# Performance work log

Measured on AMD Instinct MI355X. Metric: run time of the kernel, lower is better.

The kernel has to match this reference:

```python
import jax, jax.numpy as jnp
import numpy as np

CELL = 16          # pixels_per_cell
ORI = 6            # orientations
BIN_W = 180.0 / ORI
EPS = 1e-5         # skimage block-norm eps


def setup_inputs() -> dict:
    key = jax.random.key(0)
    x = jax.random.normal(key, (32, 3, 512, 512), dtype=jnp.float32)
    return {"x": x}


def _hog(x):
    # x: (B, 3, H, W) -> per-image HOG feature vector, matching skimage.feature.hog
    img = jnp.transpose(x, (0, 2, 3, 1))
    gray = 0.299 * img[..., 0] + 0.587 * img[..., 1] + 0.114 * img[..., 2]  # (B,H,W)
    B, H, W = gray.shape

    # skimage central-difference gradients with zeroed borders
    g_row = jnp.zeros_like(gray).at[:, 1:-1, :].set(gray[:, 2:, :] - gray[:, :-2, :])
    g_col = jnp.zeros_like(gray).at[:, :, 1:-1].set(gray[:, :, 2:] - gray[:, :, :-2])

    mag = jnp.hypot(g_row, g_col)
    ori = jnp.degrees(jnp.arctan2(g_row, g_col)) % 180.0
    bins = jnp.clip(jnp.floor(ori / BIN_W).astype(jnp.int32), 0, ORI - 1)

    # hard-assigned orientation histogram per 16x16 cell, averaged over cell pixels
    weighted = jax.nn.one_hot(bins, ORI, dtype=mag.dtype) * mag[..., None]  # (B,H,W,ORI)
    ncr, ncc = H // CELL, W // CELL
    cells = weighted.reshape(B, ncr, CELL, ncc, CELL, ORI).sum(axis=(2, 4)) / (CELL * CELL)

    # 2x2-cell blocks with stride 1 cell: (B, nbr, nbc, 2, 2, ORI)
    blocks = jnp.stack(
        [jnp.stack([cells[:, :-1, :-1], cells[:, :-1, 1:]], axis=3),
         jnp.stack([cells[:, 1:, :-1], cells[:, 1:, 1:]], axis=3)],
        axis=3)

    # L2-Hys normalization
    n1 = jnp.sqrt(jnp.sum(blocks * blocks, axis=(3, 4, 5), keepdims=True) + EPS * EPS)
    nb = jnp.minimum(blocks / n1, 0.2)
    n2 = jnp.sqrt(jnp.sum(nb * nb, axis=(3, 4, 5), keepdims=True) + EPS * EPS)
    nb = nb / n2
    return nb.reshape(B, -1).astype(jnp.float32)


def reference(x):
    return _hog(x)
```

## Files before the change

kernel.cpp:

```cpp
#include <hip/hip_runtime.h>
#include <math.h>

#define BATCH 32
#define HH 512
#define WW 512
#define NC 32
#define NORI 6
#define CH 262144

__device__ __forceinline__ int bin_of(float a) {
    const float deg = __fmul_rn(a, 57.29577951308232f);
    float m = fmodf(deg, 180.0f);
    if (m < 0.0f) m = __fadd_rn(m, 180.0f);
    const int b = (int)floorf(__fdiv_rn(m, 30.0f));
    return min(max(b, 0), NORI - 1);
}
__device__ __forceinline__ float ulp_step(float x, int k) {
    const int i = __float_as_int(x);
    int key = (i >= 0) ? i : -(i & 0x7FFFFFFF);
    key += k;
    const int r = (key >= 0) ? key : (int)(0x80000000u | (unsigned)(-key));
    return __int_as_float(r);
}
__device__ __forceinline__ void deposit(float acc[NORI], int bin, float val) {
#pragma unroll
    for (int o = 0; o < NORI; ++o) acc[o] += (bin == o) ? val : 0.0f;
}
__device__ __forceinline__ float gray_i(const float* __restrict__ img, int off) {
    return __fadd_rn(__fadd_rn(__fmul_rn(0.299f, img[off]),
                               __fmul_rn(0.587f, img[off + CH])),
                     __fmul_rn(0.114f, img[off + 2 * CH]));
}

__global__ __launch_bounds__(256) void hog_cells_kernel(const float* __restrict__ x,
                                                        float* __restrict__ cells) {
    const int b = blockIdx.z;
    const int tid = threadIdx.x;
    const int wave = tid >> 6, lane = tid & 63;
    const int R0 = blockIdx.y * 64 + wave * 16;
    const int cbase = blockIdx.x * 64;
    const int c = cbase + lane;
    const float* img = x + (size_t)b * 3 * HH * WW;

    const bool is_edge = (lane == 0) || (lane == 63);
    int hc = (lane == 0) ? (cbase - 1) : (cbase + 64);
    hc = min(max(hc, 0), WW - 1);

    float gm1 = gray_i(img, max(R0 - 1, 0) * WW + c);
    float g0  = gray_i(img, R0 * WW + c);
    float hcur = is_edge ? gray_i(img, R0 * WW + hc) : 0.0f;

    const float CC = 0.86602540378443864676f, SS = 0.5f, EPS = 1e-5f;
    const bool col_ok = (c >= 1) && (c < WW - 1);
    float acc[NORI] = {0, 0, 0, 0, 0, 0};
    unsigned ambmask = 0;

#pragma unroll
    for (int k = 0; k < 16; ++k) {
        const int r = R0 + k;
        const int rn = min(r + 1, HH - 1);
        const float gp1 = gray_i(img, rn * WW + c);
        const float hnext = is_edge ? gray_i(img, rn * WW + hc) : 0.0f;

        const bool row_ok = (r >= 1) && (r < HH - 1);
        const float gy = row_ok ? __fsub_rn(gp1, gm1) : 0.0f;
        float gl = __shfl(g0, (lane + 63) & 63);
        float gr = __shfl(g0, (lane + 1) & 63);
        if (lane == 0)  gl = hcur;
        if (lane == 63) gr = hcur;
        const float gx = col_ok ? __fsub_rn(gr, gl) : 0.0f;

        const float mag = __fsqrt_rn(__fmaf_rn(gy, gy, __fmul_rn(gx, gx)));
        const bool neg = gy < 0.0f;
        const float cy = fabsf(gy);
        const float cx = neg ? -gx : gx;
        const float t1 = __fmaf_rn(cy, CC, -__fmul_rn(cx, SS));
        const float t2 = __fmaf_rn(cy, SS, -__fmul_rn(cx, CC));
        const float t3 = -cx;
        const float t4 = __fmaf_rn(cy, -SS, -__fmul_rn(cx, CC));
        const float t5 = __fmaf_rn(cy, -CC, -__fmul_rn(cx, SS));
        int bin = (t1 >= 0.0f) + (t2 >= 0.0f) + (t3 >= 0.0f) +
                  (t4 >= 0.0f) + (t5 >= 0.0f);
        const float s = __fmul_rn(mag, EPS);
        const float mn = fminf(fminf(fminf(fabsf(t1), fabsf(t2)),
                                     fminf(fabsf(t3), fabsf(t4))), fabsf(t5));
        bool amb = (mn < s) || (cx < 0.0f && cy < s);
        if (gy == 0.0f) { bin = 0; amb = false; }
        else if (gx == 0.0f) { bin = 3; amb = false; }

        ambmask |= amb ? (1u << k) : 0u;
        deposit(acc, bin, amb ? 0.0f : mag);

        gm1 = g0; g0 = gp1; hcur = hnext;
    }

    if (__any(ambmask != 0)) {
        unsigned m = ambmask;
        while (m) {
            const int k = __builtin_ctz(m);
            m &= m - 1;
            const int r = R0 + k;
            const int off = r * WW + c;
            const float gy = __fsub_rn(gray_i(img, off + WW), gray_i(img, off - WW));
            const float gx = __fsub_rn(gray_i(img, off + 1), gray_i(img, off - 1));
            const float mag = __fsqrt_rn(__fmaf_rn(gy, gy, __fmul_rn(gx, gx)));
            const float a = atan2f(gy, gx);
            const int bl = bin_of(ulp_step(a, -2));
            const int bh = bin_of(ulp_step(a, +2));
            if (bl == bh) {
                deposit(acc, bl, mag);
            } else {
                const int b0 = bin_of(a);
                const int bo = (b0 == bl) ? bh : bl;
                deposit(acc, b0, __fmul_rn(mag, 0.65f));
                deposit(acc, bo, __fmul_rn(mag, 0.35f));
            }
        }
    }

#pragma unroll
    for (int o = 0; o < NORI; ++o) {
        float v = acc[o];
        v += __shfl_xor(v, 1);
        v += __shfl_xor(v, 2);
        v += __shfl_xor(v, 4);
        v += __shfl_xor(v, 8);
        acc[o] = v;
    }
    if ((lane & 15) == 0) {
        const int cell_r = R0 >> 4;
        const int cell_c = (cbase >> 4) + (lane >> 4);
        float* cp = cells + (((size_t)b * NC + cell_r) * NC + cell_c) * NORI;
#pragma unroll
        for (int o = 0; o < NORI; ++o) cp[o] = acc[o] * (1.0f / 256.0f);
    }
}

__global__ __launch_bounds__(256) void hog_norm_kernel(const float* __restrict__ cells,
                                                       float* __restrict__ out) {
    const int idx = blockIdx.x * 256 + threadIdx.x;
    const int total = BATCH * 31 * 31;
    if (idx >= total) return;
    const int bc = idx % 31;
    const int t = idx / 31;
    const int br = t % 31;
    const int b = t / 31;

    const float* cb = cells + (size_t)b * NC * NC * NORI;
    const float2* p0 = (const float2*)(cb + ((br) * NC + bc) * NORI);
    const float2* p1 = (const float2*)(cb + ((br + 1) * NC + bc) * NORI);
    float v[24];
#pragma unroll
    for (int q = 0; q < 6; ++q) {
        const float2 r0 = p0[q], r1 = p1[q];
        v[2 * q] = r0.x; v[2 * q + 1] = r0.y;
        v[12 + 2 * q] = r1.x; v[12 + 2 * q + 1] = r1.y;
    }
    float ss = 0.0f;
#pragma unroll
    for (int k = 0; k < 24; ++k) ss = __fadd_rn(ss, __fmul_rn(v[k], v[k]));
    const float n1 = __fsqrt_rn(__fadd_rn(ss, 1e-10f));
    float ss2 = 0.0f;
#pragma unroll
    for (int k = 0; k < 24; ++k) {
        v[k] = fminf(__fdiv_rn(v[k], n1), 0.2f);
        ss2 = __fadd_rn(ss2, __fmul_rn(v[k], v[k]));
    }
    const float n2 = __fsqrt_rn(__fadd_rn(ss2, 1e-10f));
    float* op = out + (size_t)idx * 24;
#pragma unroll
    for (int k = 0; k < 24; ++k) op[k] = __fdiv_rn(v[k], n2);
}

extern "C" void kernel_launch(void* const* d_in, const int* in_sizes, int n_in,
                              void* d_out, int out_size, void* d_ws, size_t ws_size,
                              hipStream_t stream) {
    const float* x = (const float*)d_in[0];
    float* out = (float*)d_out;
    float* cells = (float*)d_ws;

    dim3 g1(8, 8, BATCH), b1(256);
    hog_cells_kernel<<<g1, b1, 0, stream>>>(x, cells);

    const int total = BATCH * 31 * 31;
    hog_norm_kernel<<<(total + 255) / 256, 256, 0, stream>>>(cells, out);
}
```

Before: 153.2 us.

## Vectorize gray loads to float4 and retile cells with shared-memory reduction

Each lane now handles 4 adjacent columns and loads RGB through float4. Each block covers one 16-row cell row across 256 columns, with each wave taking 4 rows. Per-cell histograms are reduced with shared-memory atomics instead of a full 16-row per-wave loop, and the grid changes to 2x32xB. This widens global loads and shortens the serial row loop, at the cost of shared atomics, an extra sync, and more halo row loads per output (two extra rows for every four).

```diff
diff --git a/kernel.cpp b/kernel.cpp
--- a/kernel.cpp
+++ b/kernel.cpp
@@ -26,10 +26,50 @@
 #pragma unroll
     for (int o = 0; o < NORI; ++o) acc[o] += (bin == o) ? val : 0.0f;
 }
+__device__ __forceinline__ float gray_comb(float r, float g, float b) {
+    return __fadd_rn(__fadd_rn(__fmul_rn(0.299f, r), __fmul_rn(0.587f, g)),
+                     __fmul_rn(0.114f, b));
+}
 __device__ __forceinline__ float gray_i(const float* __restrict__ img, int off) {
-    return __fadd_rn(__fadd_rn(__fmul_rn(0.299f, img[off]),
-                               __fmul_rn(0.587f, img[off + CH])),
-                     __fmul_rn(0.114f, img[off + 2 * CH]));
+    return gray_comb(img[off], img[off + CH], img[off + 2 * CH]);
+}
+__device__ __forceinline__ float4 gray4(const float* __restrict__ img, int off) {
+    const float4 r = *(const float4*)(img + off);
+    const float4 g = *(const float4*)(img + off + CH);
+    const float4 b = *(const float4*)(img + off + 2 * CH);
+    float4 o;
+    o.x = gray_comb(r.x, g.x, b.x);
+    o.y = gray_comb(r.y, g.y, b.y);
+    o.z = gray_comb(r.z, g.z, b.z);
+    o.w = gray_comb(r.w, g.w, b.w);
+    return o;
+}
+
+__device__ __forceinline__ void hot_pixel(float gy, float gx, int bitk,
+                                          float acc[NORI], unsigned& ambmask) {
+    const float mag = __fsqrt_rn(__fmaf_rn(gy, gy, __fmul_rn(gx, gx)));
+    const bool neg = gy < 0.0f;
+    const float cy = fabsf(gy);
+    const float cx = neg ? -gx : gx;
+    const float pa = __fmul_rn(cy, 0.86602540378443864676f);
+    const float pb = __fmul_rn(cx, 0.5f);
+    const float pc = __fmul_rn(cy, 0.5f);
+    const float pd = __fmul_rn(cx, 0.86602540378443864676f);
+    const float t1 = __fsub_rn(pa, pb);
+    const float t2 = __fsub_rn(pc, pd);
+    const float t3 = -cx;
+    const float t4 = -__fadd_rn(pc, pd);
+    const float t5 = -__fadd_rn(pa, pb);
+    int bin = (t1 >= 0.0f) + (t2 >= 0.0f) + (t3 >= 0.0f) +
+              (t4 >= 0.0f) + (t5 >= 0.0f);
+    const float s = __fmul_rn(mag, 1e-5f);
+    const float mn = fminf(fminf(fminf(fabsf(t1), fabsf(t2)),
+                                 fminf(fabsf(t3), fabsf(t4))), fabsf(t5));
+    bool amb = (mn < s) || (cx < 0.0f && cy < s);
+    if (gy == 0.0f) { bin = 0; amb = false; }
+    else if (gx == 0.0f) { bin = 3; amb = false; }
+    ambmask |= amb ? (1u << bitk) : 0u;
+    deposit(acc, bin, amb ? 0.0f : mag);
 }
 
 __global__ __launch_bounds__(256) void hog_cells_kernel(const float* __restrict__ x,
@@ -37,59 +77,55 @@
     const int b = blockIdx.z;
     const int tid = threadIdx.x;
     const int wave = tid >> 6, lane = tid & 63;
-    const int R0 = blockIdx.y * 64 + wave * 16;
-    const int cbase = blockIdx.x * 64;
-    const int c = cbase + lane;
+    const int by = blockIdx.y;
+    const int R0 = by * 16 + wave * 4;
+    const int C0 = blockIdx.x * 256;
+    const int c0 = C0 + lane * 4;
     const float* img = x + (size_t)b * 3 * HH * WW;
 
-    const bool is_edge = (lane == 0) || (lane == 63);
-    int hc = (lane == 0) ? (cbase - 1) : (cbase + 64);
-    hc = min(max(hc, 0), WW - 1);
-
-    float gm1 = gray_i(img, max(R0 - 1, 0) * WW + c);
-    float g0  = gray_i(img, R0 * WW + c);
-    float hcur = is_edge ? gray_i(img, R0 * WW + hc) : 0.0f;
-
-    const float CC = 0.86602540378443864676f, SS = 0.5f, EPS = 1e-5f;
-    const bool col_ok = (c >= 1) && (c < WW - 1);
+    __shared__ float hist[16][NORI];
+    if (tid < 16 * NORI) ((float*)hist)[tid] = 0.0f;
+    __syncthreads();
+
+    const bool left_blk = (blockIdx.x == 0);
+    const int hc = left_blk ? 256 : 255;
+    const bool is_h = (lane == (left_blk ? 63 : 0));
+
+    float4 gm1 = gray4(img, max(R0 - 1, 0) * WW + c0);
+    float4 g0  = gray4(img, R0 * WW + c0);
+    float hcur = is_h ? gray_i(img, R0 * WW + hc) : 0.0f;
+
     float acc[NORI] = {0, 0, 0, 0, 0, 0};
     unsigned ambmask = 0;
 
 #pragma unroll
-    for (int k = 0; k < 16; ++k) {
+    for (int k = 0; k < 4; ++k) {
         const int r = R0 + k;
         const int rn = min(r + 1, HH - 1);
-        const float gp1 = gray_i(img, rn * WW + c);
-        const float hnext = is_edge ? gray_i(img, rn * WW + hc) : 0.0f;
+        const float4 gp1 = gray4(img, rn * WW + c0);
+        const float hnext = is_h ? gray_i(img, rn * WW + hc) : 0.0f;
 
         const bool row_ok = (r >= 1) && (r < HH - 1);
-        const float gy = row_ok ? __fsub_rn(gp1, gm1) : 0.0f;
-        float gl = __shfl(g0, (lane + 63) & 63);
-        float gr = __shfl(g0, (lane + 1) & 63);
-        if (lane == 0)  gl = hcur;
-        if (lane == 63) gr = hcur;
-        const float gx = col_ok ? __fsub_rn(gr, gl) : 0.0f;
-
-        const float mag = __fsqrt_rn(__fmaf_rn(gy, gy, __fmul_rn(gx, gx)));
-        const bool neg = gy < 0.0f;
-        const float cy = fabsf(gy);
-        const float cx = neg ? -gx : gx;
-        const float t1 = __fmaf_rn(cy, CC, -__fmul_rn(cx, SS));
-        const float t2 = __fmaf_rn(cy, SS, -__fmul_rn(cx, CC));
-        const float t3 = -cx;
-        const float t4 = __fmaf_rn(cy, -SS, -__fmul_rn(cx, CC));
-        const float t5 = __fmaf_rn(cy, -CC, -__fmul_rn(cx, SS));
-        int bin = (t1 >= 0.0f) + (t2 >= 0.0f) + (t3 >= 0.0f) +
-                  (t4 >= 0.0f) + (t5 >= 0.0f);
-        const float s = __fmul_rn(mag, EPS);
-        const float mn = fminf(fminf(fminf(fabsf(t1), fabsf(t2)),
-                                     fminf(fabsf(t3), fabsf(t4))), fabsf(t5));
-        bool amb = (mn < s) || (cx < 0.0f && cy < s);
-        if (gy == 0.0f) { bin = 0; amb = false; }
-        else if (gx == 0.0f) { bin = 3; amb = false; }
-
-        ambmask |= amb ? (1u << k) : 0u;
-        deposit(acc, bin, amb ? 0.0f : mag);
+        const float gy0 = row_ok ? __fsub_rn(gp1.x, gm1.x) : 0.0f;
+        const float gy1 = row_ok ? __fsub_rn(gp1.y, gm1.y) : 0.0f;
+        const float gy2 = row_ok ? __fsub_rn(gp1.z, gm1.z) : 0.0f;
+        const float gy3 = row_ok ? __fsub_rn(gp1.w, gm1.w) : 0.0f;
+
+        float left  = __shfl(g0.w, (lane + 63) & 63);
+        float right = __shfl(g0.x, (lane + 1) & 63);
+        if (is_h) { if (left_blk) right = hcur; else left = hcur; }
+
+        float gx0 = __fsub_rn(g0.y, left);
+        const float gx1 = __fsub_rn(g0.z, g0.x);
+        const float gx2 = __fsub_rn(g0.w, g0.y);
+        float gx3 = __fsub_rn(right, g0.z);
+        if (c0 == 0) gx0 = 0.0f;
+        if (c0 + 3 == WW - 1) gx3 = 0.0f;
+
+        hot_pixel(gy0, gx0, 4 * k + 0, acc, ambmask);
+        hot_pixel(gy1, gx1, 4 * k + 1, acc, ambmask);
+        hot_pixel(gy2, gx2, 4 * k + 2, acc, ambmask);
+        hot_pixel(gy3, gx3, 4 * k + 3, acc, ambmask);
 
         gm1 = g0; g0 = gp1; hcur = hnext;
     }
@@ -97,9 +133,10 @@
     if (__any(ambmask != 0)) {
         unsigned m = ambmask;
         while (m) {
-            const int k = __builtin_ctz(m);
+            const int bit = __builtin_ctz(m);
             m &= m - 1;
-            const int r = R0 + k;
+            const int r = R0 + (bit >> 2);
+            const int c = c0 + (bit & 3);
             const int off = r * WW + c;
             const float gy = __fsub_rn(gray_i(img, off + WW), gray_i(img, off - WW));
             const float gx = __fsub_rn(gray_i(img, off + 1), gray_i(img, off - 1));
@@ -123,16 +160,18 @@
         float v = acc[o];
         v += __shfl_xor(v, 1);
         v += __shfl_xor(v, 2);
-        v += __shfl_xor(v, 4);
-        v += __shfl_xor(v, 8);
         acc[o] = v;
     }
-    if ((lane & 15) == 0) {
-        const int cell_r = R0 >> 4;
-        const int cell_c = (cbase >> 4) + (lane >> 4);
-        float* cp = cells + (((size_t)b * NC + cell_r) * NC + cell_c) * NORI;
-#pragma unroll
-        for (int o = 0; o < NORI; ++o) cp[o] = acc[o] * (1.0f / 256.0f);
+    if ((lane & 3) == 0) {
+        const int cell = lane >> 2;
+#pragma unroll
+        for (int o = 0; o < NORI; ++o) atomicAdd(&hist[cell][o], acc[o]);
+    }
+    __syncthreads();
+    if (tid < 96) {
+        const int cell = tid / 6, o = tid - cell * 6;
+        cells[(((size_t)b * NC + by) * NC + ((C0 >> 4) + cell)) * NORI + o] =
+            hist[cell][o] * (1.0f / 256.0f);
     }
 }
 
@@ -179,7 +218,7 @@
     float* out = (float*)d_out;
     float* cells = (float*)d_ws;
 
-    dim3 g1(8, 8, BATCH), b1(256);
+    dim3 g1(2, NC, BATCH), b1(256);
     hog_cells_kernel<<<g1, b1, 0, stream>>>(x, cells);
 
     const int total = BATCH * 31 * 31;
```

New measurement: 152.8 us. Within noise of the previous version (-0.3%).
